# Kernel optimization log

Hardware: AMD Instinct MI355X
Metric: run time of the kernel (lower is better)

The kernel has to match this reference:

```python
import jax, jax.numpy as jnp
import numpy as np
import math

FEAT_SIZE = 15
DECAY = 0.92

def _decay_mask(feat_size=FEAT_SIZE, decay=DECAY):
    # coordinates of a feat_size x feat_size grid, flattened row-major ('ij' indexing like torch.meshgrid)
    xs, ys = jnp.meshgrid(jnp.arange(feat_size), jnp.arange(feat_size), indexing='ij')
    coords = jnp.stack((xs, ys), axis=-1).reshape(-1, 2)  # [HW, 2]
    dx = jnp.abs(coords[:, 0][:, None] - coords[:, 0][None, :]).astype(jnp.float32)
    dy = jnp.abs(coords[:, 1][:, None] - coords[:, 1][None, :]).astype(jnp.float32)
    return (decay ** dx) * (decay ** dy)  # [HW, HW]

def setup_inputs() -> dict:
    key = jax.random.key(0)
    k1, k2, k3, k4 = jax.random.split(key, 4)
    B, C, VD, H, W = 512, 256, 256, FEAT_SIZE, FEAT_SIZE
    centers = H * W  # 225, must match decay mask
    return {
        'm_in': jax.random.normal(k1, (B, centers, C), dtype=jnp.float32),
        'm_out': jax.random.normal(k2, (B, centers, VD), dtype=jnp.float32),
        'q_in': jax.random.normal(k3, (B, C, H, W), dtype=jnp.float32),
        'q_out': jax.random.normal(k4, (B, VD, H, W), dtype=jnp.float32),
    }

def reference(m_in, m_out, q_in, q_out):
    B, C, H, W = q_in.shape
    _, centers, _ = m_in.shape
    _, _, vd = m_out.shape
    mask = _decay_mask()  # [HW, HW] == [centers, HW]
    qi = q_in.reshape(B, C, H * W)                      # [B, C, HW]
    # scores: [B, centers, HW], scaled and multiplicatively decayed
    p = jnp.einsum('bnc,bcm->bnm', m_in, qi) / math.sqrt(C)
    p = p * mask[None, :, :]
    p = jax.nn.softmax(p, axis=1)                       # softmax over centers
    mem = jnp.einsum('bnv,bnm->bvm', m_out, p)          # [B, vd, HW]
    mem = mem.reshape(B, vd, H, W)
    mem_out = jnp.concatenate([mem, q_out], axis=1)     # [B, vd+vd2, H, W]
    return (mem_out, p)
```

## Files before the change

kernel.cpp:

```cpp
#include <hip/hip_runtime.h>


typedef float  f32x4 __attribute__((ext_vector_type(4)));
typedef short  s16x8 __attribute__((ext_vector_type(8)));
typedef unsigned short u16;
typedef u16    u16x4 __attribute__((ext_vector_type(4)));
typedef unsigned int   u32;

constexpr int   BB = 512, HW = 225, CC = 256;
constexpr float L2DECAY = -0.12029423371771177f;
constexpr float L2E     = 1.4426950408889634f;
constexpr size_t MEMOUT_PER_B = (size_t)512 * HW;
constexpr size_t P_BASE       = (size_t)BB * MEMOUT_PER_B;
constexpr size_t P_PER_B      = (size_t)HW * HW;
constexpr int SR = 72;

__device__ __forceinline__ int swz(int bid, int nb) {
    return (bid & 7) * (nb >> 3) + (bid >> 3);
}
__device__ __forceinline__ u16 f2bf(float x) {
    u32 u = __builtin_bit_cast(u32, x);
    u += 0x7fff + ((u >> 16) & 1);
    return (u16)(u >> 16);
}

__global__ __launch_bounds__(512, 4) void k1_mfma(
    const float* __restrict__ m_in, const float* __restrict__ q_in,
    float* __restrict__ out)
{
    __shared__ u16 As[256 * SR];
    __shared__ u16 Bs[128 * SR];
    __shared__ float red[4][128];

    const int bid  = swz((int)blockIdx.x, 1024);
    const int b    = bid >> 1, half = bid & 1;
    const int mB0  = half * 128;
    const int tid  = threadIdx.x, lane = tid & 63, wid = tid >> 6;
    const int wr   = wid & 3, wc = wid >> 2;
    const int l15  = lane & 15, lg = lane >> 4;

    const float* mi = m_in + (size_t)b * HW * CC;
    const float* qi = q_in + (size_t)b * CC * HW;

    f32x4 acc[4][4];
    #pragma unroll
    for (int i = 0; i < 4; ++i)
        #pragma unroll
        for (int j = 0; j < 4; ++j) acc[i][j] = {0.f, 0.f, 0.f, 0.f};

    const int abase = (wr * 64 + l15) * SR + lg * 8;
    const int bbase = (wc * 64 + l15) * SR + lg * 8;

    for (int c0 = 0; c0 < CC; c0 += 64) {
        __syncthreads();
        #pragma unroll
        for (int it = 0; it < 8; ++it) {
            const int f = it * 512 + tid, n = f >> 4, k4 = f & 15;
            float4 x = {0.f, 0.f, 0.f, 0.f};
            if (n < HW) x = *(const float4*)(mi + (size_t)n * CC + c0 + k4 * 4);
            u16x4 h = { f2bf(x.x), f2bf(x.y), f2bf(x.z), f2bf(x.w) };
            *(u16x4*)&As[n * SR + k4 * 4] = h;
        }
        #pragma unroll
        for (int it = 0; it < 4; ++it) {
            const int f = it * 512 + tid, ml = f & 127, c4 = f >> 7;
            const int m = mB0 + ml, c = c0 + c4 * 4;
            float x0 = 0.f, x1 = 0.f, x2 = 0.f, x3 = 0.f;
            if (m < HW) {
                x0 = qi[(size_t)(c + 0) * HW + m];
                x1 = qi[(size_t)(c + 1) * HW + m];
                x2 = qi[(size_t)(c + 2) * HW + m];
                x3 = qi[(size_t)(c + 3) * HW + m];
            }
            u16x4 h = { f2bf(x0), f2bf(x1), f2bf(x2), f2bf(x3) };
            *(u16x4*)&Bs[ml * SR + c4 * 4] = h;
        }
        __syncthreads();
        #pragma unroll
        for (int ks = 0; ks < 2; ++ks) {
            s16x8 a[4];
            #pragma unroll
            for (int fr = 0; fr < 4; ++fr)
                a[fr] = *(const s16x8*)&As[abase + fr * 16 * SR + ks * 32];
            #pragma unroll
            for (int fc = 0; fc < 4; ++fc) {
                const s16x8 bq = *(const s16x8*)&Bs[bbase + fc * 16 * SR + ks * 32];
                #pragma unroll
                for (int fr = 0; fr < 4; ++fr)
                    acc[fr][fc] = __builtin_amdgcn_mfma_f32_16x16x32_bf16(
                        a[fr], bq, acc[fr][fc], 0, 0, 0);
            }
        }
    }

    float mx[4];
    #pragma unroll
    for (int fc = 0; fc < 4; ++fc) {
        const int m   = mB0 + wc * 64 + fc * 16 + l15;
        const int mgx = m / 15, mgy = m % 15;
        float cmx = -3.0e38f;
        #pragma unroll
        for (int fr = 0; fr < 4; ++fr)
            #pragma unroll
            for (int r = 0; r < 4; ++r) {
                const int n = wr * 64 + fr * 16 + lg * 4 + r;
                float s;
                if (n < HW) {
                    int dx = n / 15 - mgx; dx = dx < 0 ? -dx : dx;
                    int dy = n % 15 - mgy; dy = dy < 0 ? -dy : dy;
                    s = acc[fr][fc][r] * 0.0625f * exp2f((float)(dx + dy) * L2DECAY);
                } else s = -3.0e38f;
                acc[fr][fc][r] = s;
                cmx = fmaxf(cmx, s);
            }
        cmx = fmaxf(cmx, __shfl_xor(cmx, 16));
        cmx = fmaxf(cmx, __shfl_xor(cmx, 32));
        mx[fc] = cmx;
    }
    if (lane < 16) {
        #pragma unroll
        for (int fc = 0; fc < 4; ++fc) red[wr][wc * 64 + fc * 16 + lane] = mx[fc];
    }
    __syncthreads();
    #pragma unroll
    for (int fc = 0; fc < 4; ++fc) {
        const int col = wc * 64 + fc * 16 + l15;
        mx[fc] = fmaxf(fmaxf(red[0][col], red[1][col]), fmaxf(red[2][col], red[3][col]));
    }
    __syncthreads();
    float sm[4];
    #pragma unroll
    for (int fc = 0; fc < 4; ++fc) {
        float s = 0.f;
        #pragma unroll
        for (int fr = 0; fr < 4; ++fr)
            #pragma unroll
            for (int r = 0; r < 4; ++r) {
                const float e = exp2f((acc[fr][fc][r] - mx[fc]) * L2E);
                acc[fr][fc][r] = e;
                s += e;
            }
        s += __shfl_xor(s, 16);
        s += __shfl_xor(s, 32);
        sm[fc] = s;
    }
    if (lane < 16) {
        #pragma unroll
        for (int fc = 0; fc < 4; ++fc) red[wr][wc * 64 + fc * 16 + lane] = sm[fc];
    }
    __syncthreads();
    float* pout = out + P_BASE + (size_t)b * P_PER_B;
    #pragma unroll
    for (int fc = 0; fc < 4; ++fc) {
        const int col = wc * 64 + fc * 16 + l15;
        const float inv = 1.f / (red[0][col] + red[1][col] + red[2][col] + red[3][col]);
        const int m = mB0 + wc * 64 + fc * 16 + l15;
        if (m < HW) {
            #pragma unroll
            for (int fr = 0; fr < 4; ++fr)
                #pragma unroll
                for (int r = 0; r < 4; ++r) {
                    const int n = wr * 64 + fr * 16 + lg * 4 + r;
                    if (n < HW) pout[(size_t)n * HW + m] = acc[fr][fc][r] * inv;
                }
        }
    }
}

__global__ __launch_bounds__(512, 4) void k2_mfma(
    const float* __restrict__ m_out, float* __restrict__ out)
{
    __shared__ u16 As[256 * SR];
    __shared__ u16 Bs[128 * SR];

    const int bid  = swz((int)blockIdx.x, 1024);
    const int b    = bid >> 1, half = bid & 1;
    const int mB0  = half * 128;
    const int tid  = threadIdx.x, lane = tid & 63, wid = tid >> 6;
    const int vr   = wid & 3, wc = wid >> 2;
    const int l15  = lane & 15, lg = lane >> 4;

    const float* mo = m_out + (size_t)b * HW * CC;
    const float* pb = out + P_BASE + (size_t)b * P_PER_B;

    f32x4 acc[4][4];
    #pragma unroll
    for (int i = 0; i < 4; ++i)
        #pragma unroll
        for (int j = 0; j < 4; ++j) acc[i][j] = {0.f, 0.f, 0.f, 0.f};

    const int abase = (vr * 64 + l15) * SR + lg * 8;
    const int bbase = (wc * 64 + l15) * SR + lg * 8;

    for (int n0 = 0; n0 < 256; n0 += 64) {
        __syncthreads();
        #pragma unroll
        for (int it = 0; it < 8; ++it) {
            const int f = it * 512 + tid, v = f & 255, n4 = f >> 8;
            const int n = n0 + n4 * 4;
            const float x0 = (n + 0 < HW) ? mo[(size_t)(n + 0) * CC + v] : 0.f;
            const float x1 = (n + 1 < HW) ? mo[(size_t)(n + 1) * CC + v] : 0.f;
            const float x2 = (n + 2 < HW) ? mo[(size_t)(n + 2) * CC + v] : 0.f;
            const float x3 = (n + 3 < HW) ? mo[(size_t)(n + 3) * CC + v] : 0.f;
            u16x4 h = { f2bf(x0), f2bf(x1), f2bf(x2), f2bf(x3) };
            *(u16x4*)&As[v * SR + n4 * 4] = h;
        }
        #pragma unroll
        for (int it = 0; it < 4; ++it) {
            const int f = it * 512 + tid, ml = f & 127, n4 = f >> 7;
            const int m = mB0 + ml, n = n0 + n4 * 4;
            float x0 = 0.f, x1 = 0.f, x2 = 0.f, x3 = 0.f;
            if (m < HW) {
                if (n + 0 < HW) x0 = pb[(size_t)(n + 0) * HW + m];
                if (n + 1 < HW) x1 = pb[(size_t)(n + 1) * HW + m];
                if (n + 2 < HW) x2 = pb[(size_t)(n + 2) * HW + m];
                if (n + 3 < HW) x3 = pb[(size_t)(n + 3) * HW + m];
            }
            u16x4 h = { f2bf(x0), f2bf(x1), f2bf(x2), f2bf(x3) };
            *(u16x4*)&Bs[ml * SR + n4 * 4] = h;
        }
        __syncthreads();
        #pragma unroll
        for (int ks = 0; ks < 2; ++ks) {
            s16x8 a[4];
            #pragma unroll
            for (int fr = 0; fr < 4; ++fr)
                a[fr] = *(const s16x8*)&As[abase + fr * 16 * SR + ks * 32];
            #pragma unroll
            for (int fc = 0; fc < 4; ++fc) {
                const s16x8 bq = *(const s16x8*)&Bs[bbase + fc * 16 * SR + ks * 32];
                #pragma unroll
                for (int fr = 0; fr < 4; ++fr)
                    acc[fr][fc] = __builtin_amdgcn_mfma_f32_16x16x32_bf16(
                        a[fr], bq, acc[fr][fc], 0, 0, 0);
            }
        }
    }

    float* ob = out + (size_t)b * MEMOUT_PER_B;
    #pragma unroll
    for (int fc = 0; fc < 4; ++fc) {
        const int m = mB0 + wc * 64 + fc * 16 + l15;
        if (m < HW) {
            #pragma unroll
            for (int fr = 0; fr < 4; ++fr)
                #pragma unroll
                for (int r = 0; r < 4; ++r) {
                    const int v = vr * 64 + fr * 16 + lg * 4 + r;
                    ob[(size_t)v * HW + m] = acc[fr][fc][r];
                }
        }
    }
}

__global__ __launch_bounds__(256) void k3_copy(
    const float4* __restrict__ q_out, float4* __restrict__ out)
{
    const size_t g = (size_t)blockIdx.x * 256 + threadIdx.x;
    const size_t b = g / 14400;
    const size_t r = g - b * 14400;
    out[b * 28800 + 14400 + r] = q_out[b * 14400 + r];
}

extern "C" void kernel_launch(void* const* d_in, const int* in_sizes, int n_in,
                              void* d_out, int out_size, void* d_ws, size_t ws_size,
                              hipStream_t stream) {
    const float* m_in  = (const float*)d_in[0];
    const float* m_out = (const float*)d_in[1];
    const float* q_in  = (const float*)d_in[2];
    const float* q_out = (const float*)d_in[3];
    float* out = (float*)d_out;

    k1_mfma<<<1024, 512, 0, stream>>>(m_in, q_in, out);
    k2_mfma<<<1024, 512, 0, stream>>>(m_out, out);
    k3_copy<<<(512 * 14400) / 256, 256, 0, stream>>>((const float4*)q_out, (float4*)out);
}
```

Measured before the change: 745.0 us.

## Double-buffer LDS tiles with register prefetch in both MFMA kernels

Both GEMM kernels now use a K-chunk of 32 and double-buffered LDS tiles. The next chunk's global loads are issued into registers before the current chunk's MFMAs and written to the alternate buffer afterwards, leaving one barrier per iteration. This is meant to hide global load latency behind matrix work. Block-to-batch mapping is also changed so consecutive batches group per XCD, and launch bounds drop to 2 blocks/CU, trading occupancy for more registers. The risks are higher register pressure and more loop iterations with smaller chunks.

```diff
diff --git a/kernel.cpp b/kernel.cpp
--- a/kernel.cpp
+++ b/kernel.cpp
@@ -13,27 +13,30 @@
 constexpr size_t MEMOUT_PER_B = (size_t)512 * HW;
 constexpr size_t P_BASE       = (size_t)BB * MEMOUT_PER_B;
 constexpr size_t P_PER_B      = (size_t)HW * HW;
-constexpr int SR = 72;
-
-__device__ __forceinline__ int swz(int bid, int nb) {
-    return (bid & 7) * (nb >> 3) + (bid >> 3);
-}
+constexpr int SR = 40;
+constexpr int KC = 32;
+
 __device__ __forceinline__ u16 f2bf(float x) {
     u32 u = __builtin_bit_cast(u32, x);
     u += 0x7fff + ((u >> 16) & 1);
     return (u16)(u >> 16);
 }
 
-__global__ __launch_bounds__(512, 4) void k1_mfma(
+__device__ __forceinline__ void decode_bid(int bid, int& b, int& half) {
+    const int xcd = bid & 7, j = bid >> 3;
+    half = j & 1;
+    b    = xcd * 64 + (j >> 1);
+}
+
+__global__ __launch_bounds__(512, 2) void k1_mfma(
     const float* __restrict__ m_in, const float* __restrict__ q_in,
     float* __restrict__ out)
 {
-    __shared__ u16 As[256 * SR];
-    __shared__ u16 Bs[128 * SR];
+    __shared__ u16 As[2][256 * SR];
+    __shared__ u16 Bs[2][128 * SR];
     __shared__ float red[4][128];
 
-    const int bid  = swz((int)blockIdx.x, 1024);
-    const int b    = bid >> 1, half = bid & 1;
+    int b, half;  decode_bid((int)blockIdx.x, b, half);
     const int mB0  = half * 128;
     const int tid  = threadIdx.x, lane = tid & 63, wid = tid >> 6;
     const int wr   = wid & 3, wc = wid >> 2;
@@ -51,46 +54,83 @@
     const int abase = (wr * 64 + l15) * SR + lg * 8;
     const int bbase = (wc * 64 + l15) * SR + lg * 8;
 
-    for (int c0 = 0; c0 < CC; c0 += 64) {
-        __syncthreads();
-        #pragma unroll
-        for (int it = 0; it < 8; ++it) {
-            const int f = it * 512 + tid, n = f >> 4, k4 = f & 15;
+    {
+        #pragma unroll
+        for (int it = 0; it < 4; ++it) {
+            const int f = it * 512 + tid, n = f >> 3, k4 = f & 7;
             float4 x = {0.f, 0.f, 0.f, 0.f};
-            if (n < HW) x = *(const float4*)(mi + (size_t)n * CC + c0 + k4 * 4);
+            if (n < HW) x = *(const float4*)(mi + (size_t)n * CC + k4 * 4);
             u16x4 h = { f2bf(x.x), f2bf(x.y), f2bf(x.z), f2bf(x.w) };
-            *(u16x4*)&As[n * SR + k4 * 4] = h;
-        }
-        #pragma unroll
-        for (int it = 0; it < 4; ++it) {
+            *(u16x4*)&As[0][n * SR + k4 * 4] = h;
+        }
+        #pragma unroll
+        for (int it = 0; it < 2; ++it) {
             const int f = it * 512 + tid, ml = f & 127, c4 = f >> 7;
-            const int m = mB0 + ml, c = c0 + c4 * 4;
+            const int m = mB0 + ml;
             float x0 = 0.f, x1 = 0.f, x2 = 0.f, x3 = 0.f;
             if (m < HW) {
-                x0 = qi[(size_t)(c + 0) * HW + m];
-                x1 = qi[(size_t)(c + 1) * HW + m];
-                x2 = qi[(size_t)(c + 2) * HW + m];
-                x3 = qi[(size_t)(c + 3) * HW + m];
+                x0 = qi[(size_t)(c4 * 4 + 0) * HW + m];
+                x1 = qi[(size_t)(c4 * 4 + 1) * HW + m];
+                x2 = qi[(size_t)(c4 * 4 + 2) * HW + m];
+                x3 = qi[(size_t)(c4 * 4 + 3) * HW + m];
             }
             u16x4 h = { f2bf(x0), f2bf(x1), f2bf(x2), f2bf(x3) };
-            *(u16x4*)&Bs[ml * SR + c4 * 4] = h;
+            *(u16x4*)&Bs[0][ml * SR + c4 * 4] = h;
+        }
+    }
+    __syncthreads();
+
+    int cur = 0;
+    for (int t = 0; t < CC / KC; ++t) {
+        const bool pf = (t < CC / KC - 1);
+        const int c0n = (t + 1) * KC;
+        float4 pa[4];
+        float  pb[8];
+        if (pf) {
+            #pragma unroll
+            for (int it = 0; it < 4; ++it) {
+                const int f = it * 512 + tid, n = f >> 3, k4 = f & 7;
+                pa[it] = {0.f, 0.f, 0.f, 0.f};
+                if (n < HW) pa[it] = *(const float4*)(mi + (size_t)n * CC + c0n + k4 * 4);
+            }
+            #pragma unroll
+            for (int it = 0; it < 2; ++it) {
+                const int f = it * 512 + tid, ml = f & 127, c4 = f >> 7;
+                const int m = mB0 + ml, c = c0n + c4 * 4;
+                #pragma unroll
+                for (int jj = 0; jj < 4; ++jj)
+                    pb[it * 4 + jj] = (m < HW) ? qi[(size_t)(c + jj) * HW + m] : 0.f;
+            }
+        }
+        s16x8 a[4];
+        #pragma unroll
+        for (int fr = 0; fr < 4; ++fr)
+            a[fr] = *(const s16x8*)&As[cur][abase + fr * 16 * SR];
+        #pragma unroll
+        for (int fc = 0; fc < 4; ++fc) {
+            const s16x8 bq = *(const s16x8*)&Bs[cur][bbase + fc * 16 * SR];
+            #pragma unroll
+            for (int fr = 0; fr < 4; ++fr)
+                acc[fr][fc] = __builtin_amdgcn_mfma_f32_16x16x32_bf16(
+                    a[fr], bq, acc[fr][fc], 0, 0, 0);
+        }
+        if (pf) {
+            #pragma unroll
+            for (int it = 0; it < 4; ++it) {
+                const int f = it * 512 + tid, n = f >> 3, k4 = f & 7;
+                u16x4 h = { f2bf(pa[it].x), f2bf(pa[it].y), f2bf(pa[it].z), f2bf(pa[it].w) };
+                *(u16x4*)&As[cur ^ 1][n * SR + k4 * 4] = h;
+            }
+            #pragma unroll
+            for (int it = 0; it < 2; ++it) {
+                const int f = it * 512 + tid, ml = f & 127, c4 = f >> 7;
+                u16x4 h = { f2bf(pb[it * 4 + 0]), f2bf(pb[it * 4 + 1]),
+                            f2bf(pb[it * 4 + 2]), f2bf(pb[it * 4 + 3]) };
+                *(u16x4*)&Bs[cur ^ 1][ml * SR + c4 * 4] = h;
+            }
         }
         __syncthreads();
-        #pragma unroll
-        for (int ks = 0; ks < 2; ++ks) {
-            s16x8 a[4];
-            #pragma unroll
-            for (int fr = 0; fr < 4; ++fr)
-                a[fr] = *(const s16x8*)&As[abase + fr * 16 * SR + ks * 32];
-            #pragma unroll
-            for (int fc = 0; fc < 4; ++fc) {
-                const s16x8 bq = *(const s16x8*)&Bs[bbase + fc * 16 * SR + ks * 32];
-                #pragma unroll
-                for (int fr = 0; fr < 4; ++fr)
-                    acc[fr][fc] = __builtin_amdgcn_mfma_f32_16x16x32_bf16(
-                        a[fr], bq, acc[fr][fc], 0, 0, 0);
-            }
-        }
+        cur ^= 1;
     }
 
     float mx[4];
@@ -167,21 +207,20 @@
     }
 }
 
-__global__ __launch_bounds__(512, 4) void k2_mfma(
+__global__ __launch_bounds__(512, 2) void k2_mfma(
     const float* __restrict__ m_out, float* __restrict__ out)
 {
-    __shared__ u16 As[256 * SR];
-    __shared__ u16 Bs[128 * SR];
-
-    const int bid  = swz((int)blockIdx.x, 1024);
-    const int b    = bid >> 1, half = bid & 1;
+    __shared__ u16 As[2][256 * SR];
+    __shared__ u16 Bs[2][128 * SR];
+
+    int b, half;  decode_bid((int)blockIdx.x, b, half);
     const int mB0  = half * 128;
     const int tid  = threadIdx.x, lane = tid & 63, wid = tid >> 6;
     const int vr   = wid & 3, wc = wid >> 2;
     const int l15  = lane & 15, lg = lane >> 4;
 
     const float* mo = m_out + (size_t)b * HW * CC;
-    const float* pb = out + P_BASE + (size_t)b * P_PER_B;
+    const float* pg = out + P_BASE + (size_t)b * P_PER_B;
 
     f32x4 acc[4][4];
     #pragma unroll
@@ -192,49 +231,91 @@
     const int abase = (vr * 64 + l15) * SR + lg * 8;
     const int bbase = (wc * 64 + l15) * SR + lg * 8;
 
-    for (int n0 = 0; n0 < 256; n0 += 64) {
+    {
+        #pragma unroll
+        for (int it = 0; it < 4; ++it) {
+            const int f = it * 512 + tid, v = f & 255, n4 = f >> 8;
+            float x[4];
+            #pragma unroll
+            for (int jj = 0; jj < 4; ++jj) {
+                const int n = n4 * 4 + jj;
+                x[jj] = (n < HW) ? mo[(size_t)n * CC + v] : 0.f;
+            }
+            u16x4 h = { f2bf(x[0]), f2bf(x[1]), f2bf(x[2]), f2bf(x[3]) };
+            *(u16x4*)&As[0][v * SR + n4 * 4] = h;
+        }
+        #pragma unroll
+        for (int it = 0; it < 2; ++it) {
+            const int f = it * 512 + tid, ml = f & 127, n4 = f >> 7;
+            const int m = mB0 + ml;
+            float x[4];
+            #pragma unroll
+            for (int jj = 0; jj < 4; ++jj) {
+                const int n = n4 * 4 + jj;
+                x[jj] = (m < HW && n < HW) ? pg[(size_t)n * HW + m] : 0.f;
+            }
+            u16x4 h = { f2bf(x[0]), f2bf(x[1]), f2bf(x[2]), f2bf(x[3]) };
+            *(u16x4*)&Bs[0][ml * SR + n4 * 4] = h;
+        }
+    }
+    __syncthreads();
+
+    int cur = 0;
+    for (int t = 0; t < 8; ++t) {
+        const bool pf = (t < 7);
+        const int n0n = (t + 1) * KC;
+        float pa[16], pb[8];
+        if (pf) {
+            #pragma unroll
+            for (int it = 0; it < 4; ++it) {
+                const int f = it * 512 + tid, v = f & 255, n4 = f >> 8;
+                #pragma unroll
+                for (int jj = 0; jj < 4; ++jj) {
+                    const int n = n0n + n4 * 4 + jj;
+                    pa[it * 4 + jj] = (n < HW) ? mo[(size_t)n * CC + v] : 0.f;
+                }
+            }
+            #pragma unroll
+            for (int it = 0; it < 2; ++it) {
+                const int f = it * 512 + tid, ml = f & 127, n4 = f >> 7;
+                const int m = mB0 + ml;
+                #pragma unroll
+                for (int jj = 0; jj < 4; ++jj) {
+                    const int n = n0n + n4 * 4 + jj;
+                    pb[it * 4 + jj] = (m < HW && n < HW) ? pg[(size_t)n * HW + m] : 0.f;
+                }
+            }
+        }
+        s16x8 a[4];
+        #pragma unroll
+        for (int fr = 0; fr < 4; ++fr)
+            a[fr] = *(const s16x8*)&As[cur][abase + fr * 16 * SR];
+        #pragma unroll
+        for (int fc = 0; fc < 4; ++fc) {
+            const s16x8 bq = *(const s16x8*)&Bs[cur][bbase + fc * 16 * SR];
+            #pragma unroll
+            for (int fr = 0; fr < 4; ++fr)
+                acc[fr][fc] = __builtin_amdgcn_mfma_f32_16x16x32_bf16(
+                    a[fr], bq, acc[fr][fc], 0, 0, 0);
+        }
+        if (pf) {
+            #pragma unroll
+            for (int it = 0; it < 4; ++it) {
+                const int f = it * 512 + tid, v = f & 255, n4 = f >> 8;
+                u16x4 h = { f2bf(pa[it * 4 + 0]), f2bf(pa[it * 4 + 1]),
+                            f2bf(pa[it * 4 + 2]), f2bf(pa[it * 4 + 3]) };
+                *(u16x4*)&As[cur ^ 1][v * SR + n4 * 4] = h;
+            }
+            #pragma unroll
+            for (int it = 0; it < 2; ++it) {
+                const int f = it * 512 + tid, ml = f & 127, n4 = f >> 7;
+                u16x4 h = { f2bf(pb[it * 4 + 0]), f2bf(pb[it * 4 + 1]),
+                            f2bf(pb[it * 4 + 2]), f2bf(pb[it * 4 + 3]) };
+                *(u16x4*)&Bs[cur ^ 1][ml * SR + n4 * 4] = h;
+            }
+        }
         __syncthreads();
-        #pragma unroll
-        for (int it = 0; it < 8; ++it) {
-            const int f = it * 512 + tid, v = f & 255, n4 = f >> 8;
-            const int n = n0 + n4 * 4;
-            const float x0 = (n + 0 < HW) ? mo[(size_t)(n + 0) * CC + v] : 0.f;
-            const float x1 = (n + 1 < HW) ? mo[(size_t)(n + 1) * CC + v] : 0.f;
-            const float x2 = (n + 2 < HW) ? mo[(size_t)(n + 2) * CC + v] : 0.f;
-            const float x3 = (n + 3 < HW) ? mo[(size_t)(n + 3) * CC + v] : 0.f;
-            u16x4 h = { f2bf(x0), f2bf(x1), f2bf(x2), f2bf(x3) };
-            *(u16x4*)&As[v * SR + n4 * 4] = h;
-        }
-        #pragma unroll
-        for (int it = 0; it < 4; ++it) {
-            const int f = it * 512 + tid, ml = f & 127, n4 = f >> 7;
-            const int m = mB0 + ml, n = n0 + n4 * 4;
-            float x0 = 0.f, x1 = 0.f, x2 = 0.f, x3 = 0.f;
-            if (m < HW) {
-                if (n + 0 < HW) x0 = pb[(size_t)(n + 0) * HW + m];
-                if (n + 1 < HW) x1 = pb[(size_t)(n + 1) * HW + m];
-                if (n + 2 < HW) x2 = pb[(size_t)(n + 2) * HW + m];
-                if (n + 3 < HW) x3 = pb[(size_t)(n + 3) * HW + m];
-            }
-            u16x4 h = { f2bf(x0), f2bf(x1), f2bf(x2), f2bf(x3) };
-            *(u16x4*)&Bs[ml * SR + n4 * 4] = h;
-        }
-        __syncthreads();
-        #pragma unroll
-        for (int ks = 0; ks < 2; ++ks) {
-            s16x8 a[4];
-            #pragma unroll
-            for (int fr = 0; fr < 4; ++fr)
-                a[fr] = *(const s16x8*)&As[abase + fr * 16 * SR + ks * 32];
-            #pragma unroll
-            for (int fc = 0; fc < 4; ++fc) {
-                const s16x8 bq = *(const s16x8*)&Bs[bbase + fc * 16 * SR + ks * 32];
-                #pragma unroll
-                for (int fr = 0; fr < 4; ++fr)
-                    acc[fr][fc] = __builtin_amdgcn_mfma_f32_16x16x32_bf16(
-                        a[fr], bq, acc[fr][fc], 0, 0, 0);
-            }
-        }
+        cur ^= 1;
     }
 
     float* ob = out + (size_t)b * MEMOUT_PER_B;
```

Measured after the change: 717.7 us. 1.04x faster.
